# Optimization experiments

Measured on AMD Instinct MI355X. Metric: run time of the kernel, lower is better.

The kernel has to match this reference:

```python
import jax, jax.numpy as jnp
import numpy as np

# dims: batch, tokens, channels, heads, head_dim, slices, context_slices, context_dim
B, N, C, H, D, G, SC, DC = 2, 32768, 256, 8, 32, 32, 64, 32
EPS_SLICE = 1e-5


def _ln(x, g, b):
    m = x.mean(-1, keepdims=True)
    v = ((x - m) ** 2).mean(-1, keepdims=True)
    return (x - m) * jax.lax.rsqrt(v + 1e-5) * g + b


def setup_inputs() -> dict:
    key = jax.random.key(0)
    ks = jax.random.split(key, 16)
    w = lambda k, s: jax.random.normal(k, s, jnp.float32) * 0.02
    return dict(
        fx=jax.random.normal(ks[0], (B, N, C), jnp.float32),
        context=jax.random.normal(ks[1], (B, H, SC, DC), jnp.float32),
        ln1_g=jnp.ones((C,), jnp.float32), ln1_b=jnp.zeros((C,), jnp.float32),
        Wfx=w(ks[2], (C, H * D)), bfx=jnp.zeros((H * D,), jnp.float32),
        Wx=w(ks[3], (C, H * D)), bx=jnp.zeros((H * D,), jnp.float32),
        Wslice=w(ks[4], (D, G)), bslice=jnp.zeros((G,), jnp.float32),
        temperature=0.5 * jnp.ones((1, H, 1, 1), jnp.float32),
        Wq=w(ks[5], (D, D)), Wk=w(ks[6], (D, D)), Wv=w(ks[7], (D, D)),
        Wcq=w(ks[8], (D, D)), bcq=jnp.zeros((D,), jnp.float32),
        Wck=w(ks[9], (DC, D)), bck=jnp.zeros((D,), jnp.float32),
        Wcv=w(ks[10], (DC, D)), bcv=jnp.zeros((D,), jnp.float32),
        state_mixing=jnp.zeros((), jnp.float32),
        Wout=w(ks[11], (H * D, C)), bout=jnp.zeros((C,), jnp.float32),
        ln2_g=jnp.ones((C,), jnp.float32), ln2_b=jnp.zeros((C,), jnp.float32),
        Wm1=w(ks[12], (C, 4 * C)), bm1=jnp.zeros((4 * C,), jnp.float32),
        Wm2=w(ks[13], (4 * C, C)), bm2=jnp.zeros((C,), jnp.float32),
    )


def reference(fx, context, ln1_g, ln1_b, Wfx, bfx, Wx, bx, Wslice, bslice,
              temperature, Wq, Wk, Wv, Wcq, bcq, Wck, bck, Wcv, bcv,
              state_mixing, Wout, bout, ln2_g, ln2_b, Wm1, bm1, Wm2, bm2):
    # --- GALE attention on pre-normed input (Transolver physics attention + cross) ---
    x = _ln(fx, ln1_g, ln1_b)
    fxm = (x @ Wfx + bfx).reshape(B, N, H, D).transpose(0, 2, 1, 3)  # b h n d
    xm = (x @ Wx + bx).reshape(B, N, H, D).transpose(0, 2, 1, 3)    # b h n d
    # slice weights: softmax over slices with learnable per-head temperature
    sw = jax.nn.softmax((xm @ Wslice + bslice) / temperature, axis=-1)  # b h n g
    norm = sw.sum(2)  # b h g
    st = jnp.einsum('bhnd,bhng->bhgd', fxm, sw) / (norm + EPS_SLICE)[..., None]
    scale = D ** -0.5
    # self-attention among slice tokens (no bias on q/k/v)
    q, k, v = st @ Wq, st @ Wk, st @ Wv
    sattn = jax.nn.softmax(jnp.einsum('bhgd,bhmd->bhgm', q, k) * scale, axis=-1)
    self_tok = jnp.einsum('bhgm,bhmd->bhgd', sattn, v)
    # cross-attention of slice tokens onto geometry/global context
    cq = st @ Wcq + bcq
    ck = context @ Wck + bck
    cv = context @ Wcv + bcv
    cattn = jax.nn.softmax(jnp.einsum('bhgd,bhsd->bhgs', cq, ck) * scale, axis=-1)
    cross_tok = jnp.einsum('bhgs,bhsd->bhgd', cattn, cv)
    # sigmoid-gated mix
    mw = jax.nn.sigmoid(state_mixing)
    ost = mw * self_tok + (1.0 - mw) * cross_tok
    # de-slice back to tokens and output-project
    out = jnp.einsum('bhgd,bhng->bhnd', ost, sw)
    out = out.transpose(0, 2, 1, 3).reshape(B, N, H * D) @ Wout + bout
    fx = fx + out  # residual 1
    # --- MLP block ---
    h = _ln(fx, ln2_g, ln2_b)
    fx = fx + (jax.nn.gelu(h @ Wm1 + bm1, approximate=False) @ Wm2 + bm2)
    return fx
```

## Files before the change

kernel.cpp:

```cpp
#include <hip/hip_runtime.h>
#include <hip/hip_bf16.h>

#define BATCH 2
#define NTOK  32768
#define CH    256
#define NH    8
#define HDIM  32
#define NG    32
#define NSC   64
#define NDC   32

typedef __attribute__((ext_vector_type(8))) short short8v;
typedef __attribute__((ext_vector_type(4))) short short4v;
typedef __attribute__((ext_vector_type(4))) float f32x4;

static __device__ __forceinline__ short f2bf(float f) {
    __hip_bfloat16 h = __float2bfloat16(f);
    return __builtin_bit_cast(short, h);
}
static __device__ __forceinline__ float bf2f(short s) {
    return __bfloat162float(__builtin_bit_cast(__hip_bfloat16, s));
}

static __device__ __forceinline__ void transpose_tile(
    const float* __restrict__ in, __hip_bfloat16* __restrict__ out,
    int K, int N, int blk, int tid)
{
    __shared__ float t[32][33];
    const int nb = N >> 5;
    const int bk = blk / nb;
    const int bn = blk % nb;
    const int c = tid & 31, r0 = tid >> 5;
    #pragma unroll
    for (int i = 0; i < 4; ++i) {
        const int r = r0 + i * 8;
        t[r][c] = in[(long)(bk * 32 + r) * N + bn * 32 + c];
    }
    __syncthreads();
    #pragma unroll
    for (int i = 0; i < 4; ++i) {
        const int r = r0 + i * 8;
        out[(long)(bn * 32 + r) * K + bk * 32 + c] = __float2bfloat16(t[c][r]);
    }
}

__global__ __launch_bounds__(256) void kconv_all(
    const float* __restrict__ Wfx, __hip_bfloat16* __restrict__ wcat,
    const float* __restrict__ Wout, __hip_bfloat16* __restrict__ woutt,
    const float* __restrict__ Wm1, __hip_bfloat16* __restrict__ w1t,
    const float* __restrict__ Wm2, __hip_bfloat16* __restrict__ w2t)
{
    const int b = blockIdx.x, tid = threadIdx.x;
    if (b < 64)            transpose_tile(Wfx,  wcat,  256, 256,  b,        tid);
    else if (b < 128)      transpose_tile(Wout, woutt, 256, 256,  b - 64,   tid);
    else if (b < 384)      transpose_tile(Wm1,  w1t,   256, 1024, b - 128,  tid);
    else                   transpose_tile(Wm2,  w2t,   1024, 256, b - 384,  tid);
}

__global__ __launch_bounds__(256) void kcomb(
    const float* __restrict__ Wx, const float* __restrict__ bx,
    const float* __restrict__ Wsl, const float* __restrict__ bsl,
    __hip_bfloat16* __restrict__ wcat2, float* __restrict__ bcomb)
{
    __shared__ float wcol[32];
    const int hc = blockIdx.x;
    const int h = hc >> 5, g = hc & 31;
    const int tid = threadIdx.x;
    if (tid < 32) wcol[tid] = Wsl[tid * 32 + g];
    __syncthreads();
    float a = 0.f;
    #pragma unroll
    for (int d = 0; d < 32; ++d) a += Wx[tid * 256 + h * 32 + d] * wcol[d];
    wcat2[(long)hc * 256 + tid] = __float2bfloat16(a);
    if (tid == 0) {
        float s = bsl[g];
        #pragma unroll
        for (int d = 0; d < 32; ++d) s += bx[h * 32 + d] * wcol[d];
        bcomb[hc] = s;
    }
}

__global__ __launch_bounds__(512, 4) void k1_mfma(
    const float* __restrict__ fx,
    const float* __restrict__ g1, const float* __restrict__ b1,
    const __hip_bfloat16* __restrict__ wcat,
    const float* __restrict__ bfx, const float* __restrict__ bcomb,
    const float* __restrict__ temp,
    __hip_bfloat16* __restrict__ fxm_o, __hip_bfloat16* __restrict__ sw_o)
{
    __shared__ __align__(16) char lds[65536];
    const int tid = threadIdx.x;
    const int lane = tid & 63, wid = tid >> 6;
    const long tok0 = (long)blockIdx.x * 64;
    const int col = lane & 15, kq = lane >> 4;
    const int swz = (col & 7) << 4;
    const int ep = ((kq * 16) ^ swz) & 48;
    const int e0 = (swz & 64) | ep;
    const int e1 = ((swz & 64) ^ 64) | ep;
    const int ab0 = col * 512 + e0, ab1 = col * 512 + e1;

    {
        const float4 gv = *reinterpret_cast<const float4*>(g1 + lane * 4);
        const float4 bv = *reinterpret_cast<const float4*>(b1 + lane * 4);
        #pragma unroll
        for (int tt = 0; tt < 8; ++tt) {
            const int r = wid * 8 + tt;
            const float4 v = *reinterpret_cast<const float4*>(fx + (tok0 + r) * 256 + lane * 4);
            float s = v.x + v.y + v.z + v.w;
            float s2 = v.x * v.x + v.y * v.y + v.z * v.z + v.w * v.w;
            #pragma unroll
            for (int off = 32; off; off >>= 1) {
                s  += __shfl_xor(s,  off);
                s2 += __shfl_xor(s2, off);
            }
            const float mean = s * (1.f / 256.f);
            const float rs = rsqrtf(s2 * (1.f / 256.f) - mean * mean + 1e-5f);
            short4v o;
            o[0] = f2bf((v.x - mean) * rs * gv.x + bv.x);
            o[1] = f2bf((v.y - mean) * rs * gv.y + bv.y);
            o[2] = f2bf((v.z - mean) * rs * gv.z + bv.z);
            o[3] = f2bf((v.w - mean) * rs * gv.w + bv.w);
            const int addr = r * 512 + ((lane * 8) ^ ((r & 7) << 4));
            *reinterpret_cast<short4v*>(lds + addr) = o;
        }
    }
    __syncthreads();

    const int n0 = wid * 64;
    f32x4 acc[4][4];
    #pragma unroll
    for (int mt = 0; mt < 4; ++mt)
        #pragma unroll
        for (int nt = 0; nt < 4; ++nt) acc[mt][nt] = (f32x4){0.f, 0.f, 0.f, 0.f};

    const short* wp = reinterpret_cast<const short*>(wcat) + (n0 + col) * 256 + kq * 8;
    #pragma unroll 2
    for (int j = 0; j < 4; ++j) {
        short8v a0[4], a1[4];
        #pragma unroll
        for (int mt = 0; mt < 4; ++mt) {
            a0[mt] = *reinterpret_cast<const short8v*>(lds + mt * 8192 + j * 128 + ab0);
            a1[mt] = *reinterpret_cast<const short8v*>(lds + mt * 8192 + j * 128 + ab1);
        }
        #pragma unroll
        for (int nt = 0; nt < 4; ++nt) {
            const short8v b0 = *reinterpret_cast<const short8v*>(wp + nt * 4096 + j * 64);
            const short8v b1 = *reinterpret_cast<const short8v*>(wp + nt * 4096 + j * 64 + 32);
            #pragma unroll
            for (int mt = 0; mt < 4; ++mt) {
                acc[mt][nt] = __builtin_amdgcn_mfma_f32_16x16x32_bf16(a0[mt], b0, acc[mt][nt], 0, 0, 0);
                acc[mt][nt] = __builtin_amdgcn_mfma_f32_16x16x32_bf16(a1[mt], b1, acc[mt][nt], 0, 0, 0);
            }
        }
    }
    __syncthreads();

    #pragma unroll
    for (int nt = 0; nt < 4; ++nt) {
        const int c = n0 + nt * 16 + col;
        const float bb = (c < 256) ? bfx[c] : bcomb[c - 256];
        #pragma unroll
        for (int mt = 0; mt < 4; ++mt) {
            #pragma unroll
            for (int r = 0; r < 4; ++r) {
                const int row = mt * 16 + kq * 4 + r;
                const int byte = row * 1024 + ((c * 2) ^ ((row & 7) << 4));
                *reinterpret_cast<short*>(lds + byte) = f2bf(acc[mt][nt][r] + bb);
            }
        }
    }
    __syncthreads();

    #pragma unroll
    for (int it = 0; it < 4; ++it) {
        const int idx = it * 512 + tid;
        const int row = idx >> 5, ch = idx & 31;
        const short8v val = *reinterpret_cast<const short8v*>(
            lds + row * 1024 + ((ch * 16) ^ ((row & 7) << 4)));
        *reinterpret_cast<short8v*>(
            reinterpret_cast<short*>(fxm_o) + (tok0 + row) * 256 + ch * 8) = val;
    }

    {
        const int t = tid >> 3, h = tid & 7;
        const float it_ = 1.f / temp[h];
        float lg[32];
        #pragma unroll
        for (int g = 0; g < 32; ++g) {
            const int byte = t * 1024 + (((256 + h * 32 + g) * 2) ^ ((t & 7) << 4));
            lg[g] = bf2f(*reinterpret_cast<const short*>(lds + byte)) * it_;
        }
        float mx = -1e30f;
        #pragma unroll
        for (int g = 0; g < 32; ++g) mx = fmaxf(mx, lg[g]);
        float ssum = 0.f;
        #pragma unroll
        for (int g = 0; g < 32; ++g) { lg[g] = __expf(lg[g] - mx); ssum += lg[g]; }
        const float inv = 1.f / ssum;
        #pragma unroll
        for (int g = 0; g < 32; ++g) {
            const int byte = t * 1024 + (((256 + h * 32 + g) * 2) ^ ((t & 7) << 4));
            *reinterpret_cast<short*>(lds + byte) = f2bf(lg[g] * inv);
        }
    }
    __syncthreads();

    #pragma unroll
    for (int it = 0; it < 4; ++it) {
        const int idx = it * 512 + tid;
        const int row = idx >> 5, ch = idx & 31;
        const short8v val = *reinterpret_cast<const short8v*>(
            lds + row * 1024 + ((512 + ch * 16) ^ ((row & 7) << 4)));
        *reinterpret_cast<short8v*>(
            reinterpret_cast<short*>(sw_o) + (tok0 + row) * 256 + ch * 8) = val;
    }
}

__global__ __launch_bounds__(512) void k2_st_partial(
    const __hip_bfloat16* __restrict__ fxm, const __hip_bfloat16* __restrict__ sw,
    float* __restrict__ pst, float* __restrict__ pn)
{
    __shared__ float psum[8][32][32];
    __shared__ float pns[8][32];
    const int tid = threadIdx.x, wid = tid >> 6, lane = tid & 63;
    const int blk = blockIdx.x;
    const int bh = blk >> 5, chunk = blk & 31;
    const int b = bh >> 3, h = bh & 7;
    const long rbase = (long)b * NTOK + (long)chunk * 1024 + wid * 128;
    const int gB = lane >> 3, dB = lane & 7;
    const short* sp = reinterpret_cast<const short*>(sw) + rbase * 256 + h * 32 + gB * 4;
    const short* fp = reinterpret_cast<const short*>(fxm) + rbase * 256 + h * 32 + dB * 4;

    float acc[4][4];
    float nacc[4];
    #pragma unroll
    for (int i = 0; i < 4; ++i) {
        nacc[i] = 0.f;
        #pragma unroll
        for (int j = 0; j < 4; ++j) acc[i][j] = 0.f;
    }

    #pragma unroll 4
    for (int r = 0; r < 128; ++r) {
        const short4v s4 = *reinterpret_cast<const short4v*>(sp + r * 256);
        const short4v f4 = *reinterpret_cast<const short4v*>(fp + r * 256);
        float sg[4], fd[4];
        #pragma unroll
        for (int i = 0; i < 4; ++i) { sg[i] = bf2f(s4[i]); fd[i] = bf2f(f4[i]); }
        #pragma unroll
        for (int gg = 0; gg < 4; ++gg) {
            nacc[gg] += sg[gg];
            #pragma unroll
            for (int dd = 0; dd < 4; ++dd) acc[gg][dd] += sg[gg] * fd[dd];
        }
    }

    #pragma unroll
    for (int gg = 0; gg < 4; ++gg) {
        #pragma unroll
        for (int dd = 0; dd < 4; ++dd)
            psum[wid][gB * 4 + gg][dB * 4 + dd] = acc[gg][dd];
        if (dB == 0) pns[wid][gB * 4 + gg] = nacc[gg];
    }
    __syncthreads();

    for (int i = tid; i < 1024; i += 512) {
        const int g = i >> 5, d = i & 31;
        float s = 0.f;
        #pragma unroll
        for (int w = 0; w < 8; ++w) s += psum[w][g][d];
        pst[(long)blk * 1024 + i] = s;
    }
    if (tid < 32) {
        float s = 0.f;
        #pragma unroll
        for (int w = 0; w < 8; ++w) s += pns[w][tid];
        pn[blk * 32 + tid] = s;
    }
}

__global__ __launch_bounds__(256) void k3_slice_attn(
    const float* __restrict__ pst, const float* __restrict__ pn,
    const float* __restrict__ ctx,
    const float* __restrict__ Wq, const float* __restrict__ Wk, const float* __restrict__ Wv,
    const float* __restrict__ Wcq, const float* __restrict__ bcq,
    const float* __restrict__ Wck, const float* __restrict__ bck,
    const float* __restrict__ Wcv, const float* __restrict__ bcv,
    const float* __restrict__ mix, __hip_bfloat16* __restrict__ ostT_o)
{
    __shared__ float st[1024], qm[1024], km[1024], vm[1024], cqm[1024];
    __shared__ float ckm[2048], cvm[2048], attn[2048], stok[1024], nb[32];
    const int tid = threadIdx.x;
    const int bh = blockIdx.x;

    if (tid < 32) {
        float s = 0.f;
        for (int c = 0; c < 32; ++c) s += pn[(bh * 32 + c) * 32 + tid];
        nb[tid] = s;
    }
    __syncthreads();
    for (int i = tid; i < 1024; i += 256) {
        float s = 0.f;
        for (int c = 0; c < 32; ++c) s += pst[(long)(bh * 32 + c) * 1024 + i];
        st[i] = s / (nb[i >> 5] + 1e-5f);
    }
    __syncthreads();

    for (int i = tid; i < 1024; i += 256) {
        const int g = i >> 5, d = i & 31;
        float aq = 0.f, ak = 0.f, av = 0.f, ac = bcq[d];
        #pragma unroll
        for (int e = 0; e < 32; ++e) {
            const float s = st[g * 32 + e];
            aq += s * Wq[e * 32 + d];
            ak += s * Wk[e * 32 + d];
            av += s * Wv[e * 32 + d];
            ac += s * Wcq[e * 32 + d];
        }
        qm[i] = aq; km[i] = ak; vm[i] = av; cqm[i] = ac;
    }
    const float* cbp = ctx + (long)bh * (NSC * NDC);
    for (int i = tid; i < 2048; i += 256) {
        const int s_ = i >> 5, d = i & 31;
        float w1 = bck[d], w2 = bcv[d];
        #pragma unroll
        for (int e = 0; e < 32; ++e) {
            const float cval = cbp[s_ * 32 + e];
            w1 += cval * Wck[e * 32 + d];
            w2 += cval * Wcv[e * 32 + d];
        }
        ckm[i] = w1; cvm[i] = w2;
    }
    __syncthreads();

    const float scale = 0.17677669529663687f;
    for (int i = tid; i < 1024; i += 256) {
        const int g = i >> 5, m = i & 31;
        float a = 0.f;
        #pragma unroll
        for (int d = 0; d < 32; ++d) a += qm[g * 32 + d] * km[m * 32 + d];
        attn[i] = a * scale;
    }
    __syncthreads();
    if (tid < 32) {
        float mx = -1e30f;
        for (int m = 0; m < 32; ++m) mx = fmaxf(mx, attn[tid * 32 + m]);
        float s = 0.f;
        for (int m = 0; m < 32; ++m) { const float e = expf(attn[tid * 32 + m] - mx); attn[tid * 32 + m] = e; s += e; }
        const float inv = 1.f / s;
        for (int m = 0; m < 32; ++m) attn[tid * 32 + m] *= inv;
    }
    __syncthreads();
    for (int i = tid; i < 1024; i += 256) {
        const int g = i >> 5, d = i & 31;
        float a = 0.f;
        #pragma unroll
        for (int m = 0; m < 32; ++m) a += attn[g * 32 + m] * vm[m * 32 + d];
        stok[i] = a;
    }
    __syncthreads();
    for (int i = tid; i < 2048; i += 256) {
        const int g = i >> 6, s_ = i & 63;
        float a = 0.f;
        #pragma unroll
        for (int d = 0; d < 32; ++d) a += cqm[g * 32 + d] * ckm[s_ * 32 + d];
        attn[i] = a * scale;
    }
    __syncthreads();
    if (tid < 32) {
        float mx = -1e30f;
        for (int m = 0; m < 64; ++m) mx = fmaxf(mx, attn[tid * 64 + m]);
        float s = 0.f;
        for (int m = 0; m < 64; ++m) { const float e = expf(attn[tid * 64 + m] - mx); attn[tid * 64 + m] = e; s += e; }
        const float inv = 1.f / s;
        for (int m = 0; m < 64; ++m) attn[tid * 64 + m] *= inv;
    }
    __syncthreads();
    const float mw = 1.f / (1.f + expf(-mix[0]));
    for (int i = tid; i < 1024; i += 256) {
        const int g = i >> 5, d = i & 31;
        float a = 0.f;
        #pragma unroll
        for (int s_ = 0; s_ < 64; ++s_) a += attn[g * 64 + s_] * cvm[s_ * 32 + d];
        const float val = mw * stok[i] + (1.f - mw) * a;
        ostT_o[(long)bh * 1024 + d * 32 + g] = __float2bfloat16(val);
    }
}

__global__ __launch_bounds__(512, 4) void k45_fused(
    const __hip_bfloat16* __restrict__ sw, const __hip_bfloat16* __restrict__ ostT,
    const __hip_bfloat16* __restrict__ woutt, const float* __restrict__ bout,
    const float* __restrict__ fx,
    const float* __restrict__ g2, const float* __restrict__ b2,
    const __hip_bfloat16* __restrict__ w1t, const float* __restrict__ bm1,
    const __hip_bfloat16* __restrict__ w2t, const float* __restrict__ bm2,
    float* __restrict__ out)
{
    __shared__ __align__(16) char lds[65536];
    const int tid = threadIdx.x;
    const int lane = tid & 63, wid = tid >> 6;
    const long tok0 = (long)blockIdx.x * 64;
    const int b = (int)(tok0 >> 15);
    const int col = lane & 15, kq = lane >> 4;
    const int swz = (col & 7) << 4;
    const int ep = ((kq * 16) ^ swz) & 48;
    const int e0 = (swz & 64) | ep;
    const int e1 = ((swz & 64) ^ 64) | ep;
    const int ab0 = col * 512 + e0, ab1 = col * 512 + e1;
    const int cb0 = col * 256 + e0, cb1 = col * 256 + e1;

    #pragma unroll
    for (int it = 0; it < 4; ++it) {
        const int idx = it * 512 + tid;
        const int row = idx >> 5, ch = idx & 31;
        const short8v val = *reinterpret_cast<const short8v*>(
            reinterpret_cast<const short*>(sw) + (tok0 + row) * 256 + ch * 8);
        *reinterpret_cast<short8v*>(lds + row * 512 + ((ch * 16) ^ ((row & 7) << 4))) = val;
    }
    __syncthreads();

    {
        f32x4 accal[4][2];
        const int abh = col * 512 + (((wid * 64) | (kq * 16)) ^ swz);
        short8v a[4];
        #pragma unroll
        for (int mt = 0; mt < 4; ++mt)
            a[mt] = *reinterpret_cast<const short8v*>(lds + mt * 8192 + abh);
        #pragma unroll
        for (int nt = 0; nt < 2; ++nt) {
            const int d = nt * 16 + col;
            const short8v bfr = *reinterpret_cast<const short8v*>(
                reinterpret_cast<const short*>(ostT) + ((b * 8 + wid) * 32 + d) * 32 + kq * 8);
            #pragma unroll
            for (int mt = 0; mt < 4; ++mt) {
                accal[mt][nt] = (f32x4){0.f, 0.f, 0.f, 0.f};
                accal[mt][nt] = __builtin_amdgcn_mfma_f32_16x16x32_bf16(
                    a[mt], bfr, accal[mt][nt], 0, 0, 0);
            }
        }
        #pragma unroll
        for (int nt = 0; nt < 2; ++nt) {
            const int cc = wid * 32 + nt * 16 + col;
            #pragma unroll
            for (int mt = 0; mt < 4; ++mt) {
                #pragma unroll
                for (int r = 0; r < 4; ++r) {
                    const int row = mt * 16 + kq * 4 + r;
                    const int byte = 32768 + row * 512 + ((cc * 2) ^ ((row & 7) << 4));
                    *reinterpret_cast<short*>(lds + byte) = f2bf(accal[mt][nt][r]);
                }
            }
        }
    }
    __syncthreads();

    f32x4 acc[4][2];
    #pragma unroll
    for (int mt = 0; mt < 4; ++mt)
        #pragma unroll
        for (int nt = 0; nt < 2; ++nt) acc[mt][nt] = (f32x4){0.f, 0.f, 0.f, 0.f};

    {
        const short* wp = reinterpret_cast<const short*>(woutt) + (wid * 32 + col) * 256 + kq * 8;
        #pragma unroll 2
        for (int j = 0; j < 4; ++j) {
            short8v a0[4], a1[4];
            #pragma unroll
            for (int mt = 0; mt < 4; ++mt) {
                a0[mt] = *reinterpret_cast<const short8v*>(lds + 32768 + mt * 8192 + j * 128 + ab0);
                a1[mt] = *reinterpret_cast<const short8v*>(lds + 32768 + mt * 8192 + j * 128 + ab1);
            }
            #pragma unroll
            for (int nt = 0; nt < 2; ++nt) {
                const short8v b0 = *reinterpret_cast<const short8v*>(wp + nt * 4096 + j * 64);
                const short8v b1 = *reinterpret_cast<const short8v*>(wp + nt * 4096 + j * 64 + 32);
                #pragma unroll
                for (int mt = 0; mt < 4; ++mt) {
                    acc[mt][nt] = __builtin_amdgcn_mfma_f32_16x16x32_bf16(a0[mt], b0, acc[mt][nt], 0, 0, 0);
                    acc[mt][nt] = __builtin_amdgcn_mfma_f32_16x16x32_bf16(a1[mt], b1, acc[mt][nt], 0, 0, 0);
                }
            }
        }
    }

    __syncthreads();
    float* lf = reinterpret_cast<float*>(lds);
    #pragma unroll
    for (int nt = 0; nt < 2; ++nt) {
        const int c = wid * 32 + nt * 16 + col;
        const float bb = bout[c];
        #pragma unroll
        for (int mt = 0; mt < 4; ++mt) {
            #pragma unroll
            for (int r = 0; r < 4; ++r) {
                const int row = mt * 16 + kq * 4 + r;
                lf[row * 256 + c] = acc[mt][nt][r] + bb;
            }
        }
    }
    __syncthreads();

    short4v aout[8];
    {
        const float4 gv = *reinterpret_cast<const float4*>(g2 + lane * 4);
        const float4 bv = *reinterpret_cast<const float4*>(b2 + lane * 4);
        #pragma unroll
        for (int tt = 0; tt < 8; ++tt) {
            const int r = wid * 8 + tt;
            const float4 l4 = *reinterpret_cast<const float4*>(lf + r * 256 + lane * 4);
            const float4 f4 = *reinterpret_cast<const float4*>(fx + (tok0 + r) * 256 + lane * 4);
            float4 oa;
            oa.x = l4.x + f4.x; oa.y = l4.y + f4.y;
            oa.z = l4.z + f4.z; oa.w = l4.w + f4.w;
            *reinterpret_cast<float4*>(out + (tok0 + r) * 256 + lane * 4) = oa;
            float s = oa.x + oa.y + oa.z + oa.w;
            float s2 = oa.x * oa.x + oa.y * oa.y + oa.z * oa.z + oa.w * oa.w;
            #pragma unroll
            for (int off = 32; off; off >>= 1) {
                s  += __shfl_xor(s,  off);
                s2 += __shfl_xor(s2, off);
            }
            const float mean = s * (1.f / 256.f);
            const float rs = rsqrtf(s2 * (1.f / 256.f) - mean * mean + 1e-5f);
            aout[tt][0] = f2bf((oa.x - mean) * rs * gv.x + bv.x);
            aout[tt][1] = f2bf((oa.y - mean) * rs * gv.y + bv.y);
            aout[tt][2] = f2bf((oa.z - mean) * rs * gv.z + bv.z);
            aout[tt][3] = f2bf((oa.w - mean) * rs * gv.w + bv.w);
        }
    }
    __syncthreads();
    #pragma unroll
    for (int tt = 0; tt < 8; ++tt) {
        const int r = wid * 8 + tt;
        const int addr = r * 512 + ((lane * 8) ^ ((r & 7) << 4));
        *reinterpret_cast<short4v*>(lds + addr) = aout[tt];
    }
    __syncthreads();

    const int n0 = wid * 32;
    const int h0 = wid * 16;
    const short* w1s = reinterpret_cast<const short*>(w1t) + (h0 + col) * 256 + kq * 8;
    const short* w2s = reinterpret_cast<const short*>(w2t) + (n0 + col) * 1024 + kq * 8;

    f32x4 accO[4][2];
    #pragma unroll
    for (int mt = 0; mt < 4; ++mt)
        #pragma unroll
        for (int nt = 0; nt < 2; ++nt) accO[mt][nt] = (f32x4){0.f, 0.f, 0.f, 0.f};

    for (int ch = 0; ch < 8; ++ch) {
        const int abuf = 32768 + (ch & 1) * 16384;

        f32x4 accP[4];
        #pragma unroll
        for (int mt = 0; mt < 4; ++mt) accP[mt] = (f32x4){0.f, 0.f, 0.f, 0.f};

        #pragma unroll 1
        for (int j = 0; j < 4; ++j) {
            const short8v b0 = *reinterpret_cast<const short8v*>(w1s + ch * 32768 + j * 64);
            const short8v b1 = *reinterpret_cast<const short8v*>(w1s + ch * 32768 + j * 64 + 32);
            #pragma unroll
            for (int mt = 0; mt < 4; ++mt) {
                const short8v a0 = *reinterpret_cast<const short8v*>(lds + mt * 8192 + j * 128 + ab0);
                const short8v a1 = *reinterpret_cast<const short8v*>(lds + mt * 8192 + j * 128 + ab1);
                accP[mt] = __builtin_amdgcn_mfma_f32_16x16x32_bf16(a0, b0, accP[mt], 0, 0, 0);
                accP[mt] = __builtin_amdgcn_mfma_f32_16x16x32_bf16(a1, b1, accP[mt], 0, 0, 0);
            }
        }

        {
            const float b1v = bm1[ch * 128 + h0 + col];
            const int k2i2 = (h0 + col) * 2;
            #pragma unroll
            for (int mt = 0; mt < 4; ++mt) {
                #pragma unroll
                for (int r = 0; r < 4; ++r) {
                    float m = accP[mt][r] + b1v;
                    const float u = __builtin_fmaf(0.044715f * m, m * m, m);
                    const float e = __expf(-1.5957691216057308f * u);
                    m = m * __builtin_amdgcn_rcpf(1.f + e);
                    const int row = mt * 16 + kq * 4 + r;
                    const int byte = abuf + row * 256 + (k2i2 ^ ((row & 7) << 4));
                    *reinterpret_cast<short*>(lds + byte) = f2bf(m);
                }
            }
        }
        __syncthreads();

        #pragma unroll 1
        for (int j = 0; j < 2; ++j) {
            short8v b20[2], b21[2];
            #pragma unroll
            for (int nt = 0; nt < 2; ++nt) {
                b20[nt] = *reinterpret_cast<const short8v*>(w2s + nt * 16384 + ch * 128 + j * 64);
                b21[nt] = *reinterpret_cast<const short8v*>(w2s + nt * 16384 + ch * 128 + j * 64 + 32);
            }
            #pragma unroll
            for (int mt = 0; mt < 4; ++mt) {
                const short8v x0 = *reinterpret_cast<const short8v*>(lds + abuf + mt * 4096 + j * 128 + cb0);
                const short8v x1 = *reinterpret_cast<const short8v*>(lds + abuf + mt * 4096 + j * 128 + cb1);
                #pragma unroll
                for (int nt = 0; nt < 2; ++nt) {
                    accO[mt][nt] = __builtin_amdgcn_mfma_f32_16x16x32_bf16(x0, b20[nt], accO[mt][nt], 0, 0, 0);
                    accO[mt][nt] = __builtin_amdgcn_mfma_f32_16x16x32_bf16(x1, b21[nt], accO[mt][nt], 0, 0, 0);
                }
            }
        }
    }

    __syncthreads();
    #pragma unroll
    for (int nt = 0; nt < 2; ++nt) {
        const int c = n0 + nt * 16 + col;
        const float b2v = bm2[c];
        #pragma unroll
        for (int mt = 0; mt < 4; ++mt) {
            #pragma unroll
            for (int r = 0; r < 4; ++r) {
                const int row = mt * 16 + kq * 4 + r;
                lf[row * 256 + c] = accO[mt][nt][r] + b2v;
            }
        }
    }
    __syncthreads();
    #pragma unroll
    for (int tt = 0; tt < 8; ++tt) {
        const int r = wid * 8 + tt;
        const float4 m4 = *reinterpret_cast<const float4*>(lf + r * 256 + lane * 4);
        const long gidx = (tok0 + r) * 256 + lane * 4;
        const float4 oa = *reinterpret_cast<const float4*>(out + gidx);
        float4 o;
        o.x = oa.x + m4.x; o.y = oa.y + m4.y;
        o.z = oa.z + m4.z; o.w = oa.w + m4.w;
        *reinterpret_cast<float4*>(out + gidx) = o;
    }
}

extern "C" void kernel_launch(void* const* d_in, const int* in_sizes, int n_in,
                              void* d_out, int out_size, void* d_ws, size_t ws_size,
                              hipStream_t stream)
{
    const float* fx   = (const float*)d_in[0];
    const float* ctx  = (const float*)d_in[1];
    const float* g1   = (const float*)d_in[2];
    const float* b1   = (const float*)d_in[3];
    const float* Wfx  = (const float*)d_in[4];
    const float* bfx  = (const float*)d_in[5];
    const float* Wx   = (const float*)d_in[6];
    const float* bx   = (const float*)d_in[7];
    const float* Wsl  = (const float*)d_in[8];
    const float* bsl  = (const float*)d_in[9];
    const float* temp = (const float*)d_in[10];
    const float* Wq   = (const float*)d_in[11];
    const float* Wk   = (const float*)d_in[12];
    const float* Wv   = (const float*)d_in[13];
    const float* Wcq  = (const float*)d_in[14];
    const float* bcq  = (const float*)d_in[15];
    const float* Wck  = (const float*)d_in[16];
    const float* bck  = (const float*)d_in[17];
    const float* Wcv  = (const float*)d_in[18];
    const float* bcv  = (const float*)d_in[19];
    const float* mix  = (const float*)d_in[20];
    const float* Wout = (const float*)d_in[21];
    const float* bout = (const float*)d_in[22];
    const float* g2   = (const float*)d_in[23];
    const float* b2   = (const float*)d_in[24];
    const float* Wm1  = (const float*)d_in[25];
    const float* bm1  = (const float*)d_in[26];
    const float* Wm2  = (const float*)d_in[27];
    const float* bm2  = (const float*)d_in[28];
    float* out = (float*)d_out;

    char* ws = (char*)d_ws;
    __hip_bfloat16* fxm  = (__hip_bfloat16*)ws;
    __hip_bfloat16* sw   = (__hip_bfloat16*)(ws + (size_t)33554432);
    float* pst = (float*)(ws + (size_t)67108864);
    float* pn  = (float*)(ws + (size_t)69206016);
    __hip_bfloat16* ostT  = (__hip_bfloat16*)(ws + (size_t)69271552);
    __hip_bfloat16* wcat  = (__hip_bfloat16*)(ws + (size_t)69304320);
    __hip_bfloat16* woutt = (__hip_bfloat16*)(ws + (size_t)69566464);
    __hip_bfloat16* w1t   = (__hip_bfloat16*)(ws + (size_t)69697536);
    __hip_bfloat16* w2t   = (__hip_bfloat16*)(ws + (size_t)70221824);
    float* bcomb          = (float*)(ws + (size_t)70746112);

    kconv_all<<<640, 256, 0, stream>>>(Wfx, wcat, Wout, woutt, Wm1, w1t, Wm2, w2t);
    kcomb<<<256, 256, 0, stream>>>(Wx, bx, Wsl, bsl, wcat + 65536, bcomb);

    k1_mfma<<<1024, 512, 0, stream>>>(fx, g1, b1, wcat, bfx, bcomb, temp,
                                      fxm, sw);
    k2_st_partial<<<512, 512, 0, stream>>>(fxm, sw, pst, pn);
    k3_slice_attn<<<16, 256, 0, stream>>>(pst, pn, ctx, Wq, Wk, Wv,
                                          Wcq, bcq, Wck, bck, Wcv, bcv, mix, ostT);
    k45_fused<<<1024, 512, 0, stream>>>(sw, ostT, woutt, bout, fx,
                                        g2, b2, w1t, bm1, w2t, bm2, out);
}
```

Baseline: 312.5 us.

## Merge weight-prep kernels and restructure slice-token partial reduction

The two weight-preparation kernels become one launch. The slice-token partial kernel is reorganised so each block covers 256 tokens for all heads, one wave per head. Each wave writes its partial sums straight to global memory, which drops the shared-memory cross-wave reduction and the block barrier. The partials now reuse the fxm workspace region that the block has just read, and the slice-attention kernel sums 128 partials per head instead of 32. The cost is more serial work in the tiny 16-block reduction kernel, plus a possible read/write race on the aliased workspace between waves of the same block.

```diff
diff --git a/kernel.cpp b/kernel.cpp
--- a/kernel.cpp
+++ b/kernel.cpp
@@ -44,34 +44,29 @@
     }
 }
 
-__global__ __launch_bounds__(256) void kconv_all(
+__global__ __launch_bounds__(256) void kprep(
     const float* __restrict__ Wfx, __hip_bfloat16* __restrict__ wcat,
     const float* __restrict__ Wout, __hip_bfloat16* __restrict__ woutt,
     const float* __restrict__ Wm1, __hip_bfloat16* __restrict__ w1t,
-    const float* __restrict__ Wm2, __hip_bfloat16* __restrict__ w2t)
+    const float* __restrict__ Wm2, __hip_bfloat16* __restrict__ w2t,
+    const float* __restrict__ Wx, const float* __restrict__ bx,
+    const float* __restrict__ Wsl, const float* __restrict__ bsl,
+    float* __restrict__ bcomb)
 {
     const int b = blockIdx.x, tid = threadIdx.x;
-    if (b < 64)            transpose_tile(Wfx,  wcat,  256, 256,  b,        tid);
-    else if (b < 128)      transpose_tile(Wout, woutt, 256, 256,  b - 64,   tid);
-    else if (b < 384)      transpose_tile(Wm1,  w1t,   256, 1024, b - 128,  tid);
-    else                   transpose_tile(Wm2,  w2t,   1024, 256, b - 384,  tid);
-}
-
-__global__ __launch_bounds__(256) void kcomb(
-    const float* __restrict__ Wx, const float* __restrict__ bx,
-    const float* __restrict__ Wsl, const float* __restrict__ bsl,
-    __hip_bfloat16* __restrict__ wcat2, float* __restrict__ bcomb)
-{
+    if (b < 64)       { transpose_tile(Wfx,  wcat,  256, 256,  b,       tid); return; }
+    else if (b < 128) { transpose_tile(Wout, woutt, 256, 256,  b - 64,  tid); return; }
+    else if (b < 384) { transpose_tile(Wm1,  w1t,   256, 1024, b - 128, tid); return; }
+    else if (b < 640) { transpose_tile(Wm2,  w2t,   1024, 256, b - 384, tid); return; }
     __shared__ float wcol[32];
-    const int hc = blockIdx.x;
+    const int hc = b - 640;
     const int h = hc >> 5, g = hc & 31;
-    const int tid = threadIdx.x;
     if (tid < 32) wcol[tid] = Wsl[tid * 32 + g];
     __syncthreads();
     float a = 0.f;
     #pragma unroll
     for (int d = 0; d < 32; ++d) a += Wx[tid * 256 + h * 32 + d] * wcol[d];
-    wcat2[(long)hc * 256 + tid] = __float2bfloat16(a);
+    (wcat + 65536)[(long)hc * 256 + tid] = __float2bfloat16(a);
     if (tid == 0) {
         float s = bsl[g];
         #pragma unroll
@@ -217,19 +212,16 @@
 }
 
 __global__ __launch_bounds__(512) void k2_st_partial(
-    const __hip_bfloat16* __restrict__ fxm, const __hip_bfloat16* __restrict__ sw,
-    float* __restrict__ pst, float* __restrict__ pn)
+    const __hip_bfloat16* fxm, const __hip_bfloat16* sw,
+    float* pst)
 {
-    __shared__ float psum[8][32][32];
-    __shared__ float pns[8][32];
     const int tid = threadIdx.x, wid = tid >> 6, lane = tid & 63;
-    const int blk = blockIdx.x;
-    const int bh = blk >> 5, chunk = blk & 31;
-    const int b = bh >> 3, h = bh & 7;
-    const long rbase = (long)b * NTOK + (long)chunk * 1024 + wid * 128;
+    const int bc = blockIdx.x;
+    const long tb = (long)bc * 256;
+    const int h = wid;
     const int gB = lane >> 3, dB = lane & 7;
-    const short* sp = reinterpret_cast<const short*>(sw) + rbase * 256 + h * 32 + gB * 4;
-    const short* fp = reinterpret_cast<const short*>(fxm) + rbase * 256 + h * 32 + dB * 4;
+    const short* sp = reinterpret_cast<const short*>(sw) + tb * 256 + h * 32 + gB * 4;
+    const short* fp = reinterpret_cast<const short*>(fxm) + tb * 256 + h * 32 + dB * 4;
 
     float acc[4][4];
     float nacc[4];
@@ -241,7 +233,7 @@
     }
 
     #pragma unroll 4
-    for (int r = 0; r < 128; ++r) {
+    for (int r = 0; r < 256; ++r) {
         const short4v s4 = *reinterpret_cast<const short4v*>(sp + r * 256);
         const short4v f4 = *reinterpret_cast<const short4v*>(fp + r * 256);
         float sg[4], fd[4];
@@ -255,32 +247,22 @@
         }
     }
 
+    float* po = pst + (long)bc * 32768 + h * 1024;
     #pragma unroll
     for (int gg = 0; gg < 4; ++gg) {
         #pragma unroll
         for (int dd = 0; dd < 4; ++dd)
-            psum[wid][gB * 4 + gg][dB * 4 + dd] = acc[gg][dd];
-        if (dB == 0) pns[wid][gB * 4 + gg] = nacc[gg];
-    }
-    __syncthreads();
-
-    for (int i = tid; i < 1024; i += 512) {
-        const int g = i >> 5, d = i & 31;
-        float s = 0.f;
-        #pragma unroll
-        for (int w = 0; w < 8; ++w) s += psum[w][g][d];
-        pst[(long)blk * 1024 + i] = s;
-    }
-    if (tid < 32) {
-        float s = 0.f;
-        #pragma unroll
-        for (int w = 0; w < 8; ++w) s += pns[w][tid];
-        pn[blk * 32 + tid] = s;
+            po[(gB * 4 + gg) * 32 + dB * 4 + dd] = acc[gg][dd];
+    }
+    if (dB == 0) {
+        float* pno = pst + (long)bc * 32768 + 8192 + h * 32;
+        #pragma unroll
+        for (int gg = 0; gg < 4; ++gg) pno[gB * 4 + gg] = nacc[gg];
     }
 }
 
 __global__ __launch_bounds__(256) void k3_slice_attn(
-    const float* __restrict__ pst, const float* __restrict__ pn,
+    const float* __restrict__ pst,
     const float* __restrict__ ctx,
     const float* __restrict__ Wq, const float* __restrict__ Wk, const float* __restrict__ Wv,
     const float* __restrict__ Wcq, const float* __restrict__ bcq,
@@ -292,16 +274,21 @@
     __shared__ float ckm[2048], cvm[2048], attn[2048], stok[1024], nb[32];
     const int tid = threadIdx.x;
     const int bh = blockIdx.x;
+    const int b = bh >> 3, h = bh & 7;
 
     if (tid < 32) {
         float s = 0.f;
-        for (int c = 0; c < 32; ++c) s += pn[(bh * 32 + c) * 32 + tid];
+        #pragma unroll 4
+        for (int c = 0; c < 128; ++c)
+            s += pst[(long)(b * 128 + c) * 32768 + 8192 + h * 32 + tid];
         nb[tid] = s;
     }
     __syncthreads();
     for (int i = tid; i < 1024; i += 256) {
         float s = 0.f;
-        for (int c = 0; c < 32; ++c) s += pst[(long)(bh * 32 + c) * 1024 + i];
+        #pragma unroll 4
+        for (int c = 0; c < 128; ++c)
+            s += pst[(long)(b * 128 + c) * 32768 + h * 1024 + i];
         st[i] = s / (nb[i >> 5] + 1e-5f);
     }
     __syncthreads();
@@ -674,8 +661,7 @@
     char* ws = (char*)d_ws;
     __hip_bfloat16* fxm  = (__hip_bfloat16*)ws;
     __hip_bfloat16* sw   = (__hip_bfloat16*)(ws + (size_t)33554432);
-    float* pst = (float*)(ws + (size_t)67108864);
-    float* pn  = (float*)(ws + (size_t)69206016);
+    float* pst = (float*)ws;
     __hip_bfloat16* ostT  = (__hip_bfloat16*)(ws + (size_t)69271552);
     __hip_bfloat16* wcat  = (__hip_bfloat16*)(ws + (size_t)69304320);
     __hip_bfloat16* woutt = (__hip_bfloat16*)(ws + (size_t)69566464);
@@ -683,13 +669,13 @@
     __hip_bfloat16* w2t   = (__hip_bfloat16*)(ws + (size_t)70221824);
     float* bcomb          = (float*)(ws + (size_t)70746112);
 
-    kconv_all<<<640, 256, 0, stream>>>(Wfx, wcat, Wout, woutt, Wm1, w1t, Wm2, w2t);
-    kcomb<<<256, 256, 0, stream>>>(Wx, bx, Wsl, bsl, wcat + 65536, bcomb);
+    kprep<<<896, 256, 0, stream>>>(Wfx, wcat, Wout, woutt, Wm1, w1t, Wm2, w2t,
+                                   Wx, bx, Wsl, bsl, bcomb);
 
     k1_mfma<<<1024, 512, 0, stream>>>(fx, g1, b1, wcat, bfx, bcomb, temp,
                                       fxm, sw);
-    k2_st_partial<<<512, 512, 0, stream>>>(fxm, sw, pst, pn);
-    k3_slice_attn<<<16, 256, 0, stream>>>(pst, pn, ctx, Wq, Wk, Wv,
+    k2_st_partial<<<256, 512, 0, stream>>>(fxm, sw, pst);
+    k3_slice_attn<<<16, 256, 0, stream>>>(pst, ctx, Wq, Wk, Wv,
                                           Wcq, bcq, Wck, bck, Wcv, bcv, mix, ostT);
     k45_fused<<<1024, 512, 0, stream>>>(sw, ostT, woutt, bout, fx,
                                         g2, b2, w1t, bm1, w2t, bm2, out);
```

Result: slower. 343.5 us (+9.9%).
